# Kernel optimization log

Hardware: AMD Instinct MI355X
Metric: run time of the kernel (lower is better)

## Reference

```python
import jax, jax.numpy as jnp
import numpy as np

NUM_ENTITIES = 100000
NUM_RELATIONS = 500
DIM = 512
CHANNELS = 32
KERNEL = 3
BATCH = 2048


def setup_inputs() -> dict:
    key = jax.random.key(0)
    ks = jax.random.split(key, 9)
    # xavier_uniform bounds
    b_ent = float(np.sqrt(6.0 / (NUM_ENTITIES + DIM)))
    b_rel = float(np.sqrt(6.0 / (NUM_RELATIONS + DIM)))
    ent = jax.random.uniform(ks[0], (NUM_ENTITIES, DIM), jnp.float32, -b_ent, b_ent)
    rel = jax.random.uniform(ks[1], (NUM_RELATIONS, DIM), jnp.float32, -b_rel, b_rel)
    # Conv1d(1, CHANNELS, KERNEL) default init: U(-s, s), s = 1/sqrt(in_ch*k)
    s_conv = float(1.0 / np.sqrt(1 * KERNEL))
    conv_w = jax.random.uniform(ks[2], (CHANNELS, 1, KERNEL), jnp.float32, -s_conv, s_conv)
    conv_b = jax.random.uniform(ks[3], (CHANNELS,), jnp.float32, -s_conv, s_conv)
    # Linear(CHANNELS*DIM, DIM)
    s_proj = float(1.0 / np.sqrt(CHANNELS * DIM))
    proj_w = jax.random.uniform(ks[4], (DIM, CHANNELS * DIM), jnp.float32, -s_proj, s_proj)
    proj_b = jax.random.uniform(ks[5], (DIM,), jnp.float32, -s_proj, s_proj)
    h = jax.random.randint(ks[6], (BATCH,), 0, NUM_ENTITIES, jnp.int32)
    r = jax.random.randint(ks[7], (BATCH,), 0, NUM_RELATIONS, jnp.int32)
    t = jax.random.randint(ks[8], (BATCH,), 0, NUM_ENTITIES, jnp.int32)
    return {"h": h, "r": r, "t": t, "ent": ent, "rel": rel,
            "conv_w": conv_w, "conv_b": conv_b, "proj_w": proj_w, "proj_b": proj_b}


def reference(h, r, t, ent, rel, conv_w, conv_b, proj_w, proj_b):
    dim = ent.shape[1]
    h_e = ent[h]                                   # [B, D]
    r_e = rel[r]                                   # [B, D]
    x = jnp.concatenate([h_e, r_e], axis=-1)[:, None, :]   # [B, 1, 2D]
    x = jax.lax.conv_general_dilated(
        x, conv_w, window_strides=(1,), padding='SAME',
        dimension_numbers=('NCH', 'OIH', 'NCH'))   # [B, C, 2D]
    x = jax.nn.relu(x + conv_b[None, :, None])
    x = x[..., :dim]                               # [B, C, D]
    x = x.reshape(x.shape[0], -1)                  # [B, C*D]
    x = x @ proj_w.T + proj_b                      # [B, D]
    scores = x @ ent.T                             # [B, N] full-entity scores
    return scores[jnp.arange(t.shape[0]), t]       # [B]
```

## Files before the change

kernel.cpp:

```cpp
#include <hip/hip_runtime.h>

#define DIM    512
#define CH     32
#define KDIM   16384
#define BATCH  2048
#define NOUT   512
#define PWN    (NOUT * KDIM)
#define CONVBLK (PWN / 4 / 256)

#define BM 128
#define BN 128
#define BK 64
#define KSPLIT 8
#define KC (KDIM / KSPLIT)

typedef short bf16x8 __attribute__((ext_vector_type(8)));
typedef float f32x4  __attribute__((ext_vector_type(4)));

__device__ __forceinline__ float b2f(unsigned short u) {
    union { unsigned int i; float f; } v; v.i = ((unsigned int)u) << 16; return v.f;
}
__device__ __forceinline__ unsigned short f2b(float f) {
    union { float f; unsigned int i; } v; v.f = f;
    unsigned int r = v.i + 0x7fffu + ((v.i >> 16) & 1u);
    return (unsigned short)(r >> 16);
}
__device__ __forceinline__ float ldv(const void* p, size_t i, int isf) {
    return isf ? ((const float*)p)[i] : b2f(((const unsigned short*)p)[i]);
}
__device__ __forceinline__ int sniff_isf32(const unsigned short* ent_raw) {
    int lane = threadIdx.x & 63;
    unsigned short u = ent_raw[2 * lane];
    int eb = (u >> 8) & 0x7F;
    unsigned long long m = __ballot(eb >= 0x36 && eb < 0x3C);
    return (__popcll(m) < 32) ? 1 : 0;
}

__device__ __forceinline__ void gload_lds16(const unsigned short* g, unsigned short* l) {
    __builtin_amdgcn_global_load_lds(
        (const __attribute__((address_space(1))) void*)g,
        (__attribute__((address_space(3))) void*)l,
        16, 0, 0);
}

__global__ __launch_bounds__(256) void prep_kernel(
    const int* __restrict__ h, const int* __restrict__ r,
    const void* __restrict__ ent, const void* __restrict__ rel,
    const void* __restrict__ conv_w, const void* __restrict__ conv_b,
    const void* __restrict__ projw,
    unsigned short* __restrict__ pw16, unsigned short* __restrict__ feat)
{
    const int tid = threadIdx.x;
    const int isf = sniff_isf32((const unsigned short*)ent);

    if (blockIdx.x < CONVBLK) {
        size_t i0 = ((size_t)blockIdx.x * 256 + tid) * 4;
        if (isf) {
            f32x4 v = *(const f32x4*)((const float*)projw + i0);
            unsigned int p0 = (unsigned int)f2b(v[0]) | ((unsigned int)f2b(v[1]) << 16);
            unsigned int p1 = (unsigned int)f2b(v[2]) | ((unsigned int)f2b(v[3]) << 16);
            *(unsigned int*)(pw16 + i0) = p0;
            *(unsigned int*)(pw16 + i0 + 2) = p1;
        } else {
            *(unsigned long long*)(pw16 + i0) =
                *(const unsigned long long*)((const unsigned short*)projw + i0);
        }
        return;
    }

    __shared__ float xs[DIM + 2];
    __shared__ float wS[CH][4];
    const int b = blockIdx.x - CONVBLK;

    const size_t hb = (size_t)h[b] * DIM;
    for (int j = tid; j < DIM; j += 256) xs[1 + j] = ldv(ent, hb + j, isf);
    if (tid == 0) xs[0] = 0.0f;
    if (tid == 1) xs[DIM + 1] = ldv(rel, (size_t)r[b] * DIM, isf);
    if (tid >= 64 && tid < 96) {
        int c = tid - 64;
        wS[c][0] = ldv(conv_w, c * 3 + 0, isf);
        wS[c][1] = ldv(conv_w, c * 3 + 1, isf);
        wS[c][2] = ldv(conv_w, c * 3 + 2, isf);
        wS[c][3] = ldv(conv_b, c, isf);
    }
    __syncthreads();

    unsigned short* fb = feat + (size_t)b * KDIM;
    const int i0 = tid * 2;
    float x0 = xs[i0], x1 = xs[i0 + 1], x2 = xs[i0 + 2], x3 = xs[i0 + 3];
    #pragma unroll 8
    for (int c = 0; c < CH; ++c) {
        float w0 = wS[c][0], w1 = wS[c][1], w2 = wS[c][2], cb = wS[c][3];
        float v0 = fmaxf(fmaf(w0, x0, fmaf(w1, x1, fmaf(w2, x2, cb))), 0.0f);
        float v1 = fmaxf(fmaf(w0, x1, fmaf(w1, x2, fmaf(w2, x3, cb))), 0.0f);
        unsigned int pack = (unsigned int)f2b(v0) | ((unsigned int)f2b(v1) << 16);
        *(unsigned int*)&fb[c * DIM + i0] = pack;
    }
}

__global__ __launch_bounds__(256, 2) void gemm_kernel(
    const unsigned short* __restrict__ feat,
    const unsigned short* __restrict__ pw16,
    float* __restrict__ Xp)
{
    __shared__ __align__(16) unsigned short As[BM * BK];
    __shared__ __align__(16) unsigned short Bs[BN * BK];

    const int tid  = threadIdx.x;
    const int lane = tid & 63;
    const int wave = tid >> 6;
    const int wm = wave & 1;
    const int wn = wave >> 1;
    const int bx = blockIdx.x, by = blockIdx.y, bz = blockIdx.z;

    const unsigned short* Ab = feat + (size_t)(bx * BM) * KDIM + bz * KC;
    const unsigned short* Bb = pw16 + (size_t)(by * BN) * KDIM + bz * KC;

    const int row_ld = tid >> 3;
    const int koff   = (tid & 7) * 8;

    const f32x4 zero = {0.f, 0.f, 0.f, 0.f};
    f32x4 acc[4][4];
    #pragma unroll
    for (int i = 0; i < 4; ++i)
        #pragma unroll
        for (int j = 0; j < 4; ++j) acc[i][j] = zero;

    const int fRow = lane & 15;
    const int fK   = (lane >> 4) * 8;

    for (int kk = 0; kk < KC; kk += BK) {
        #pragma unroll
        for (int j = 0; j < 4; ++j) {
            int rw = row_ld + 32 * j;
            gload_lds16(Ab + (size_t)rw * KDIM + kk + koff, As + rw * BK + koff);
            gload_lds16(Bb + (size_t)rw * KDIM + kk + koff, Bs + rw * BK + koff);
        }
        __syncthreads();

        #pragma unroll
        for (int ko = 0; ko < 2; ++ko) {
            bf16x8 af[4], bfr[4];
            #pragma unroll
            for (int mi = 0; mi < 4; ++mi)
                af[mi] = *(const bf16x8*)&As[(wm * 64 + mi * 16 + fRow) * BK + ko * 32 + fK];
            #pragma unroll
            for (int ni = 0; ni < 4; ++ni)
                bfr[ni] = *(const bf16x8*)&Bs[(wn * 64 + ni * 16 + fRow) * BK + ko * 32 + fK];
            #pragma unroll
            for (int mi = 0; mi < 4; ++mi)
                #pragma unroll
                for (int ni = 0; ni < 4; ++ni)
                    acc[mi][ni] = __builtin_amdgcn_mfma_f32_16x16x32_bf16(
                        af[mi], bfr[ni], acc[mi][ni], 0, 0, 0);
        }
        __syncthreads();
    }

    float* Xs = Xp + (size_t)bz * BATCH * NOUT;
    const int rbase = bx * BM + wm * 64 + (lane >> 4) * 4;
    const int cbase = by * BN + wn * 64 + (lane & 15);
    #pragma unroll
    for (int mi = 0; mi < 4; ++mi)
        #pragma unroll
        for (int ni = 0; ni < 4; ++ni)
            #pragma unroll
            for (int rr = 0; rr < 4; ++rr) {
                int row = rbase + mi * 16 + rr;
                int col = cbase + ni * 16;
                Xs[(size_t)row * NOUT + col] = acc[mi][ni][rr];
            }
}

__global__ __launch_bounds__(256) void score_kernel(
    const int* __restrict__ t, const void* __restrict__ ent,
    const float* __restrict__ Xp, const void* __restrict__ projb,
    void* __restrict__ out)
{
    const int lane = threadIdx.x & 63;
    const int wave = threadIdx.x >> 6;
    const int b = blockIdx.x * 4 + wave;
    const int isf = sniff_isf32((const unsigned short*)ent);
    const size_t tb = (size_t)t[b] * DIM;
    float s = 0.f;
    if (isf) {
        const float* te = (const float*)ent + tb;
        const float* pb = (const float*)projb;
        const int d0 = lane * 8;
        #pragma unroll
        for (int jj = 0; jj < 2; ++jj) {
            int d = d0 + jj * 4;
            f32x4 xp = *(const f32x4*)(pb + d);
            #pragma unroll
            for (int z = 0; z < KSPLIT; ++z)
                xp += *(const f32x4*)(Xp + (size_t)z * BATCH * NOUT + (size_t)b * NOUT + d);
            f32x4 tv = *(const f32x4*)(te + d);
            s += xp[0]*tv[0] + xp[1]*tv[1] + xp[2]*tv[2] + xp[3]*tv[3];
        }
    } else {
        #pragma unroll
        for (int j = 0; j < 8; ++j) {
            int d = lane + 64 * j;
            float xp = ldv(projb, d, 0);
            #pragma unroll
            for (int z = 0; z < KSPLIT; ++z)
                xp += Xp[(size_t)z * BATCH * NOUT + (size_t)b * NOUT + d];
            s += xp * ldv(ent, tb + d, 0);
        }
    }
    #pragma unroll
    for (int o = 32; o; o >>= 1) s += __shfl_xor(s, o, 64);
    if (lane == 0) {
        if (isf) ((float*)out)[b] = s;
        else     ((unsigned short*)out)[b] = f2b(s);
    }
}

extern "C" void kernel_launch(void* const* d_in, const int* in_sizes, int n_in,
                              void* d_out, int out_size, void* d_ws, size_t ws_size,
                              hipStream_t stream)
{
    const int* h = (const int*)d_in[0];
    const int* r = (const int*)d_in[1];
    const int* t = (const int*)d_in[2];
    const void* ent    = d_in[3];
    const void* rel    = d_in[4];
    const void* conv_w = d_in[5];
    const void* conv_b = d_in[6];
    const void* projw  = d_in[7];
    const void* projb  = d_in[8];

    unsigned short* feat = (unsigned short*)d_ws;
    unsigned short* pw16 = (unsigned short*)((char*)d_ws + (size_t)BATCH * KDIM * 2);
    float* Xp = (float*)((char*)pw16 + (size_t)PWN * 2);

    prep_kernel<<<CONVBLK + BATCH, 256, 0, stream>>>(h, r, ent, rel, conv_w, conv_b,
                                                     projw, pw16, feat);
    gemm_kernel<<<dim3(BATCH / BM, NOUT / BN, KSPLIT), 256, 0, stream>>>(feat, pw16, Xp);
    score_kernel<<<BATCH / 4, 256, 0, stream>>>(t, ent, Xp, projb, d_out);
}
```

Baseline: 333.7 us.

## Rewrite GEMM as 256x256 double-buffered swizzled pipeline with deeper split-K

The GEMM kernel moves to 256x256 tiles on 512-thread blocks. It double-buffers LDS with an XOR swizzle and interleaves global-to-LDS prefetches with MFMA chunks, using explicit barriers, waitcnts and s_setprio. The goal is to hide global load latency, avoid LDS bank conflicts and raise MFMA utilisation. Split-K goes from 8 to 16 to keep all CUs busy with the larger tiles. That doubles the partial-sum workspace and the reduction reads in the score kernel, and the 128KB LDS footprint limits occupancy to one block per CU.

```diff
diff --git a/kernel.cpp b/kernel.cpp
--- a/kernel.cpp
+++ b/kernel.cpp
@@ -8,11 +8,13 @@
 #define PWN    (NOUT * KDIM)
 #define CONVBLK (PWN / 4 / 256)
 
-#define BM 128
-#define BN 128
+#define BM 256
+#define BN 256
 #define BK 64
-#define KSPLIT 8
+#define KSPLIT 16
 #define KC (KDIM / KSPLIT)
+#define NKT (KC / BK)
+#define NITER (NKT / 2)
 
 typedef short bf16x8 __attribute__((ext_vector_type(8)));
 typedef float f32x4  __attribute__((ext_vector_type(4)));
@@ -98,70 +100,148 @@
     }
 }
 
-__global__ __launch_bounds__(256, 2) void gemm_kernel(
+#define BAR()    asm volatile("s_barrier" ::: "memory")
+#define WAITL()  asm volatile("s_waitcnt lgkmcnt(0)" ::: "memory")
+#define WAITV(n) asm volatile("s_waitcnt vmcnt(" #n ")" ::: "memory")
+
+__global__ __launch_bounds__(512, 2) void gemm_kernel(
     const unsigned short* __restrict__ feat,
     const unsigned short* __restrict__ pw16,
     float* __restrict__ Xp)
 {
-    __shared__ __align__(16) unsigned short As[BM * BK];
-    __shared__ __align__(16) unsigned short Bs[BN * BK];
+    __shared__ __align__(16) unsigned short As[2][2][128][64];
+    __shared__ __align__(16) unsigned short Bs[2][2][128][64];
 
     const int tid  = threadIdx.x;
     const int lane = tid & 63;
-    const int wave = tid >> 6;
-    const int wm = wave & 1;
-    const int wn = wave >> 1;
+    const int w    = tid >> 6;
+    const int wm   = w >> 2;
+    const int wn   = w & 3;
+    const int fr   = lane & 15;
+    const int g    = lane >> 4;
+
     const int bx = blockIdx.x, by = blockIdx.y, bz = blockIdx.z;
 
-    const unsigned short* Ab = feat + (size_t)(bx * BM) * KDIM + bz * KC;
-    const unsigned short* Bb = pw16 + (size_t)(by * BN) * KDIM + bz * KC;
-
-    const int row_ld = tid >> 3;
-    const int koff   = (tid & 7) * 8;
-
+    const unsigned short* Abase = feat + (size_t)(bx * BM) * KDIM + (size_t)bz * KC;
+    const unsigned short* Bbase = pw16 + (size_t)(by * BN) * KDIM + (size_t)bz * KC;
+
+    const int r0      = tid >> 3;
+    const int kg      = (((tid & 7) ^ (r0 & 7)) << 3);
+    const int ldsoff0 = tid << 3;
+
+    const int ps0 = ((0 + g) ^ (fr & 7)) << 3;
+    const int ps1 = ((4 + g) ^ (fr & 7)) << 3;
+    const int brow = (wn & 1) * 64 + fr;
+
+    f32x4 acc[8][4];
     const f32x4 zero = {0.f, 0.f, 0.f, 0.f};
-    f32x4 acc[4][4];
     #pragma unroll
-    for (int i = 0; i < 4; ++i)
+    for (int i = 0; i < 8; ++i)
         #pragma unroll
         for (int j = 0; j < 4; ++j) acc[i][j] = zero;
 
-    const int fRow = lane & 15;
-    const int fK   = (lane >> 4) * 8;
-
-    for (int kk = 0; kk < KC; kk += BK) {
-        #pragma unroll
-        for (int j = 0; j < 4; ++j) {
-            int rw = row_ld + 32 * j;
-            gload_lds16(Ab + (size_t)rw * KDIM + kk + koff, As + rw * BK + koff);
-            gload_lds16(Bb + (size_t)rw * KDIM + kk + koff, Bs + rw * BK + koff);
-        }
-        __syncthreads();
-
-        #pragma unroll
-        for (int ko = 0; ko < 2; ++ko) {
-            bf16x8 af[4], bfr[4];
-            #pragma unroll
-            for (int mi = 0; mi < 4; ++mi)
-                af[mi] = *(const bf16x8*)&As[(wm * 64 + mi * 16 + fRow) * BK + ko * 32 + fK];
-            #pragma unroll
-            for (int ni = 0; ni < 4; ++ni)
-                bfr[ni] = *(const bf16x8*)&Bs[(wn * 64 + ni * 16 + fRow) * BK + ko * 32 + fK];
-            #pragma unroll
-            for (int mi = 0; mi < 4; ++mi)
-                #pragma unroll
-                for (int ni = 0; ni < 4; ++ni)
-                    acc[mi][ni] = __builtin_amdgcn_mfma_f32_16x16x32_bf16(
-                        af[mi], bfr[ni], acc[mi][ni], 0, 0, 0);
-        }
-        __syncthreads();
-    }
+    bf16x8 af[4][2];
+    bf16x8 bfr[4][2];
+
+#define STG(gbase, larr, t, hh) do {                                          \
+    const unsigned short* _s = (gbase) + (size_t)((hh) * 128) * KDIM          \
+                               + (size_t)((t) * BK) + kg;                     \
+    unsigned short* _l = &larr[(t) & 1][hh][0][0];                            \
+    gload_lds16(_s + (size_t)r0 * KDIM,        _l + ldsoff0);                 \
+    gload_lds16(_s + (size_t)(r0 + 64) * KDIM, _l + ldsoff0 + 4096);          \
+} while (0)
+
+#define LDA(d, m0) do {                                                       \
+    _Pragma("unroll")                                                         \
+    for (int _m = 0; _m < 4; ++_m) {                                          \
+        const unsigned short* _rp = &As[d][wm][((m0) + _m) * 16 + fr][0];     \
+        af[_m][0] = *(const bf16x8*)(_rp + ps0);                              \
+        af[_m][1] = *(const bf16x8*)(_rp + ps1);                              \
+    }                                                                         \
+} while (0)
+
+#define LDB(d, n0) do {                                                       \
+    _Pragma("unroll")                                                         \
+    for (int _n = 0; _n < 2; ++_n) {                                          \
+        const unsigned short* _rp = &Bs[d][wn >> 1][brow + ((n0) + _n) * 16][0]; \
+        bfr[(n0) + _n][0] = *(const bf16x8*)(_rp + ps0);                      \
+        bfr[(n0) + _n][1] = *(const bf16x8*)(_rp + ps1);                      \
+    }                                                                         \
+} while (0)
+
+#define MM(m0, n0) do {                                                       \
+    __builtin_amdgcn_s_setprio(1);                                            \
+    _Pragma("unroll")                                                         \
+    for (int _m = 0; _m < 4; ++_m) {                                          \
+        _Pragma("unroll")                                                     \
+        for (int _n = 0; _n < 2; ++_n) {                                      \
+            acc[(m0)+_m][(n0)+_n] = __builtin_amdgcn_mfma_f32_16x16x32_bf16(  \
+                af[_m][0], bfr[(n0)+_n][0], acc[(m0)+_m][(n0)+_n], 0, 0, 0);  \
+            acc[(m0)+_m][(n0)+_n] = __builtin_amdgcn_mfma_f32_16x16x32_bf16(  \
+                af[_m][1], bfr[(n0)+_n][1], acc[(m0)+_m][(n0)+_n], 0, 0, 0);  \
+        }                                                                     \
+    }                                                                         \
+    __builtin_amdgcn_s_setprio(0);                                            \
+} while (0)
+
+    STG(Abase, As, 0, 0); STG(Abase, As, 0, 1);
+    STG(Bbase, Bs, 0, 0); STG(Bbase, Bs, 0, 1);
+    STG(Abase, As, 1, 0); STG(Abase, As, 1, 1);
+    STG(Bbase, Bs, 1, 0); STG(Bbase, Bs, 1, 1);
+    WAITV(8);
+    BAR();
+
+    for (int i = 0; i < NITER; ++i) {
+        const int t2 = 2 * i;
+        const int more = (i + 1 < NITER);
+        LDA(0, 0); LDB(0, 0);
+        if (i > 0) { STG(Bbase, Bs, t2 + 1, 0); STG(Bbase, Bs, t2 + 1, 1); }
+        BAR(); WAITL();
+        MM(0, 0);
+        BAR();
+        LDB(0, 2);
+        BAR(); WAITL();
+        MM(0, 2);
+        BAR();
+        LDA(0, 4);
+        BAR(); WAITL();
+        MM(4, 2);
+        BAR();
+        if (more) { STG(Abase, As, t2 + 2, 0); STG(Abase, As, t2 + 2, 1); }
+        BAR(); WAITL();
+        MM(4, 0);
+        if (more) { WAITV(4); } else { WAITV(0); }
+        BAR();
+        LDA(1, 0); LDB(1, 0);
+        if (more) { STG(Bbase, Bs, t2 + 2, 0); STG(Bbase, Bs, t2 + 2, 1); }
+        BAR(); WAITL();
+        MM(0, 0);
+        BAR();
+        LDB(1, 2);
+        BAR(); WAITL();
+        MM(0, 2);
+        BAR();
+        LDA(1, 4);
+        BAR(); WAITL();
+        MM(4, 2);
+        BAR();
+        if (more) { STG(Abase, As, t2 + 3, 0); STG(Abase, As, t2 + 3, 1); }
+        BAR(); WAITL();
+        MM(4, 0);
+        if (more) { WAITV(4); } else { WAITV(0); }
+        BAR();
+    }
+
+#undef STG
+#undef LDA
+#undef LDB
+#undef MM
 
     float* Xs = Xp + (size_t)bz * BATCH * NOUT;
-    const int rbase = bx * BM + wm * 64 + (lane >> 4) * 4;
+    const int rbase = bx * BM + wm * 128 + (lane >> 4) * 4;
     const int cbase = by * BN + wn * 64 + (lane & 15);
     #pragma unroll
-    for (int mi = 0; mi < 4; ++mi)
+    for (int mi = 0; mi < 8; ++mi)
         #pragma unroll
         for (int ni = 0; ni < 4; ++ni)
             #pragma unroll
@@ -236,6 +316,6 @@
 
     prep_kernel<<<CONVBLK + BATCH, 256, 0, stream>>>(h, r, ent, rel, conv_w, conv_b,
                                                      projw, pw16, feat);
-    gemm_kernel<<<dim3(BATCH / BM, NOUT / BN, KSPLIT), 256, 0, stream>>>(feat, pw16, Xp);
+    gemm_kernel<<<dim3(BATCH / BM, NOUT / BN, KSPLIT), 512, 0, stream>>>(feat, pw16, Xp);
     score_kernel<<<BATCH / 4, 256, 0, stream>>>(t, ent, Xp, projb, d_out);
 }
```

Result: no change. 340.0 us (+1.9%).

## Fuse target-entity dot product into GEMM epilogue with atomic accumulation

Applied to the files above, without the earlier changes.

Instead of writing KSPLIT partial projection outputs to workspace and reducing them in a separate score kernel, each GEMM tile now dots its partial outputs with the gathered target embeddings, reduces across lanes, and atomically adds into the per-row score. The bias term dot product is computed in the prep kernel and written as the initial value. This removes the large fp32 partial-output write and reread, but adds gathered ent loads and atomics in the epilogue. It also makes the result order-dependent in floating point.

```diff
diff --git a/kernel.cpp b/kernel.cpp
--- a/kernel.cpp
+++ b/kernel.cpp
@@ -45,10 +45,12 @@
 
 __global__ __launch_bounds__(256) void prep_kernel(
     const int* __restrict__ h, const int* __restrict__ r,
+    const int* __restrict__ t,
     const void* __restrict__ ent, const void* __restrict__ rel,
     const void* __restrict__ conv_w, const void* __restrict__ conv_b,
-    const void* __restrict__ projw,
-    unsigned short* __restrict__ pw16, unsigned short* __restrict__ feat)
+    const void* __restrict__ projw, const void* __restrict__ projb,
+    unsigned short* __restrict__ pw16, unsigned short* __restrict__ feat,
+    float* __restrict__ acc_ws, void* __restrict__ out)
 {
     const int tid = threadIdx.x;
     const int isf = sniff_isf32((const unsigned short*)ent);
@@ -96,12 +98,30 @@
         unsigned int pack = (unsigned int)f2b(v0) | ((unsigned int)f2b(v1) << 16);
         *(unsigned int*)&fb[c * DIM + i0] = pack;
     }
+
+    if (tid >= 192) {
+        const int l = tid - 192;
+        const size_t tb = (size_t)t[b] * DIM;
+        float s = 0.f;
+        #pragma unroll
+        for (int j = 0; j < 8; ++j) {
+            int d = l + 64 * j;
+            s += ldv(projb, d, isf) * ldv(ent, tb + d, isf);
+        }
+        #pragma unroll
+        for (int o = 32; o; o >>= 1) s += __shfl_xor(s, o, 64);
+        if (l == 0) {
+            float* oacc = isf ? (float*)out : acc_ws;
+            oacc[b] = s;
+        }
+    }
 }
 
 __global__ __launch_bounds__(256, 2) void gemm_kernel(
     const unsigned short* __restrict__ feat,
     const unsigned short* __restrict__ pw16,
-    float* __restrict__ Xp)
+    const int* __restrict__ t, const void* __restrict__ ent,
+    float* __restrict__ acc_ws, void* __restrict__ out)
 {
     __shared__ __align__(16) unsigned short As[BM * BK];
     __shared__ __align__(16) unsigned short Bs[BN * BK];
@@ -112,6 +132,7 @@
     const int wm = wave & 1;
     const int wn = wave >> 1;
     const int bx = blockIdx.x, by = blockIdx.y, bz = blockIdx.z;
+    const int isf = sniff_isf32((const unsigned short*)ent);
 
     const unsigned short* Ab = feat + (size_t)(bx * BM) * KDIM + bz * KC;
     const unsigned short* Bb = pw16 + (size_t)(by * BN) * KDIM + bz * KC;
@@ -157,63 +178,37 @@
         __syncthreads();
     }
 
-    float* Xs = Xp + (size_t)bz * BATCH * NOUT;
-    const int rbase = bx * BM + wm * 64 + (lane >> 4) * 4;
-    const int cbase = by * BN + wn * 64 + (lane & 15);
+    float* oacc = isf ? (float*)out : acc_ws;
+    const int g16 = lane >> 4;
+    const int l16 = lane & 15;
+    const int rbase = bx * BM + wm * 64 + g16 * 4;
+    const int cbase = by * BN + wn * 64 + l16;
     #pragma unroll
     for (int mi = 0; mi < 4; ++mi)
         #pragma unroll
-        for (int ni = 0; ni < 4; ++ni)
-            #pragma unroll
-            for (int rr = 0; rr < 4; ++rr) {
-                int row = rbase + mi * 16 + rr;
-                int col = cbase + ni * 16;
-                Xs[(size_t)row * NOUT + col] = acc[mi][ni][rr];
-            }
-}
-
-__global__ __launch_bounds__(256) void score_kernel(
-    const int* __restrict__ t, const void* __restrict__ ent,
-    const float* __restrict__ Xp, const void* __restrict__ projb,
+        for (int rr = 0; rr < 4; ++rr) {
+            const int row = rbase + mi * 16 + rr;
+            const size_t tb = (size_t)t[row] * DIM;
+            float v = 0.f;
+            #pragma unroll
+            for (int ni = 0; ni < 4; ++ni)
+                v += acc[mi][ni][rr] * ldv(ent, tb + cbase + ni * 16, isf);
+            v += __shfl_xor(v, 1, 64);
+            v += __shfl_xor(v, 2, 64);
+            v += __shfl_xor(v, 4, 64);
+            v += __shfl_xor(v, 8, 64);
+            if (l16 == 0) atomicAdd(oacc + row, v);
+        }
+}
+
+__global__ __launch_bounds__(256) void finish_kernel(
+    const void* __restrict__ ent, const float* __restrict__ acc_ws,
     void* __restrict__ out)
 {
-    const int lane = threadIdx.x & 63;
-    const int wave = threadIdx.x >> 6;
-    const int b = blockIdx.x * 4 + wave;
     const int isf = sniff_isf32((const unsigned short*)ent);
-    const size_t tb = (size_t)t[b] * DIM;
-    float s = 0.f;
-    if (isf) {
-        const float* te = (const float*)ent + tb;
-        const float* pb = (const float*)projb;
-        const int d0 = lane * 8;
-        #pragma unroll
-        for (int jj = 0; jj < 2; ++jj) {
-            int d = d0 + jj * 4;
-            f32x4 xp = *(const f32x4*)(pb + d);
-            #pragma unroll
-            for (int z = 0; z < KSPLIT; ++z)
-                xp += *(const f32x4*)(Xp + (size_t)z * BATCH * NOUT + (size_t)b * NOUT + d);
-            f32x4 tv = *(const f32x4*)(te + d);
-            s += xp[0]*tv[0] + xp[1]*tv[1] + xp[2]*tv[2] + xp[3]*tv[3];
-        }
-    } else {
-        #pragma unroll
-        for (int j = 0; j < 8; ++j) {
-            int d = lane + 64 * j;
-            float xp = ldv(projb, d, 0);
-            #pragma unroll
-            for (int z = 0; z < KSPLIT; ++z)
-                xp += Xp[(size_t)z * BATCH * NOUT + (size_t)b * NOUT + d];
-            s += xp * ldv(ent, tb + d, 0);
-        }
-    }
-    #pragma unroll
-    for (int o = 32; o; o >>= 1) s += __shfl_xor(s, o, 64);
-    if (lane == 0) {
-        if (isf) ((float*)out)[b] = s;
-        else     ((unsigned short*)out)[b] = f2b(s);
-    }
+    if (isf) return;
+    const int b = blockIdx.x * 256 + threadIdx.x;
+    ((unsigned short*)out)[b] = f2b(acc_ws[b]);
 }
 
 extern "C" void kernel_launch(void* const* d_in, const int* in_sizes, int n_in,
@@ -232,10 +227,13 @@
 
     unsigned short* feat = (unsigned short*)d_ws;
     unsigned short* pw16 = (unsigned short*)((char*)d_ws + (size_t)BATCH * KDIM * 2);
-    float* Xp = (float*)((char*)pw16 + (size_t)PWN * 2);
-
-    prep_kernel<<<CONVBLK + BATCH, 256, 0, stream>>>(h, r, ent, rel, conv_w, conv_b,
-                                                     projw, pw16, feat);
-    gemm_kernel<<<dim3(BATCH / BM, NOUT / BN, KSPLIT), 256, 0, stream>>>(feat, pw16, Xp);
-    score_kernel<<<BATCH / 4, 256, 0, stream>>>(t, ent, Xp, projb, d_out);
-}
+    float* acc_ws = (float*)((char*)pw16 + (size_t)PWN * 2);
+
+    prep_kernel<<<CONVBLK + BATCH, 256, 0, stream>>>(h, r, t, ent, rel, conv_w, conv_b,
+                                                     projw, projb, pw16, feat,
+                                                     acc_ws, d_out);
+    gemm_kernel<<<dim3(BATCH / BM, NOUT / BN, KSPLIT), 256, 0, stream>>>(feat, pw16,
+                                                                         t, ent,
+                                                                         acc_ws, d_out);
+    finish_kernel<<<BATCH / 256, 256, 0, stream>>>(ent, acc_ws, d_out);
+}
```

New measurement: 341.6 us. 1.02x slower.
